# Optimization experiments

Hardware: AMD Instinct MI355X
Metric: run time of the kernel (lower is better)

Reference implementation:

```python
import jax, jax.numpy as jnp
import numpy as np

B, S = 4096, 32
H, NH, HD = 512, 8, 64
NL = 6            # encoder layers
E = 128           # num_experts
CTX = 32          # context_length
LN_EPS = 1e-5


def _ln(x, w, b):
    mu = jnp.mean(x, axis=-1, keepdims=True)
    var = jnp.mean((x - mu) ** 2, axis=-1, keepdims=True)
    return (x - mu) * jax.lax.rsqrt(var + LN_EPS) * w + b


def setup_inputs() -> dict:
    key = jax.random.key(0)
    ks = jax.random.split(key, 20)
    n = lambda k, shape: (jax.random.normal(k, shape, jnp.float32) * 0.02)
    return dict(
        expert_sequence=jax.random.randint(ks[0], (B, S), 0, E),
        layer_id=jax.random.randint(ks[1], (B,), 0, 12),
        expert_table=n(ks[2], (E, H)),
        layer_table=n(ks[3], (12, H)),
        pos_table=n(ks[4], (CTX, H)),
        qkv_w=n(ks[5], (NL, 3 * H, H)), qkv_b=n(ks[6], (NL, 3 * H)),
        out_w=n(ks[7], (NL, H, H)), out_b=n(ks[8], (NL, H)),
        ln1_w=jnp.ones((NL, H)), ln1_b=jnp.zeros((NL, H)),
        ff1_w=n(ks[9], (NL, 2 * H, H)), ff1_b=n(ks[10], (NL, 2 * H)),
        ff2_w=n(ks[11], (NL, H, 2 * H)), ff2_b=n(ks[12], (NL, H)),
        ln2_w=jnp.ones((NL, H)), ln2_b=jnp.zeros((NL, H)),
        head_w=n(ks[13], (NL, E, H)), head_b=n(ks[14], (NL, E)),
        conf_w=n(ks[15], (1, H)), conf_b=jnp.zeros((1,), jnp.float32),
    )


def reference(expert_sequence, layer_id, expert_table, layer_table, pos_table,
              qkv_w, qkv_b, out_w, out_b, ln1_w, ln1_b,
              ff1_w, ff1_b, ff2_w, ff2_b, ln2_w, ln2_b,
              head_w, head_b, conf_w, conf_b):
    Bn, Sn = expert_sequence.shape
    # embedding sum (position defaults to arange % context_length)
    x = (expert_table[expert_sequence]
         + layer_table[layer_id][:, None, :]
         + pos_table[jnp.arange(Sn) % CTX][None, :, :])  # [B,S,H]

    scale = 1.0 / np.float32(np.sqrt(HD))
    for i in range(NL):  # post-norm TransformerEncoderLayer, relu FFN, eval (no dropout)
        qkv = x @ qkv_w[i].T + qkv_b[i]                  # [B,S,3H]
        q, k, v = jnp.split(qkv, 3, axis=-1)
        hview = lambda t: t.reshape(Bn, Sn, NH, HD).transpose(0, 2, 1, 3)
        q, k, v = hview(q), hview(k), hview(v)           # [B,NH,S,HD]
        att = jax.nn.softmax(jnp.einsum('bhqd,bhkd->bhqk', q, k) * scale, axis=-1)
        o = jnp.einsum('bhqk,bhkd->bhqd', att, v).transpose(0, 2, 1, 3).reshape(Bn, Sn, H)
        x = _ln(x + o @ out_w[i].T + out_b[i], ln1_w[i], ln1_b[i])
        ff = jax.nn.relu(x @ ff1_w[i].T + ff1_b[i]) @ ff2_w[i].T + ff2_b[i]
        x = _ln(x + ff, ln2_w[i], ln2_b[i])

    last = x[:, -1, :]                                   # [B,H]
    # head selection: odd layers {1,3,...,11} -> heads 0..5, else fall back to head '1' (idx 0)
    head_idx = jnp.where(layer_id % 2 == 1, (layer_id - 1) // 2, 0)
    prediction = jnp.einsum('bh,beh->be', last, head_w[head_idx]) + head_b[head_idx]
    confidence = jax.nn.sigmoid(last @ conf_w.T + conf_b)  # [B,1]
    return prediction, confidence
```

## Files before the change

### kernel.cpp

```cpp
#include <hip/hip_runtime.h>

typedef __bf16 bf16;
typedef bf16 bf16x8 __attribute__((ext_vector_type(8)));
typedef bf16 bf16x4 __attribute__((ext_vector_type(4)));
typedef float f32x4 __attribute__((ext_vector_type(4)));

#define B_ 4096
#define S_ 32
#define H_ 512
#define NL_ 6
constexpr size_t TOK = (size_t)B_ * S_;

typedef __attribute__((address_space(1))) void* gas_t;
typedef __attribute__((address_space(3))) void* las_t;

__device__ __forceinline__ void async16(bf16* lds, const bf16* g) {
    __builtin_amdgcn_global_load_lds((gas_t)g, (las_t)lds, 16, 0, 0);
}

template<bool RELU>
__global__ __launch_bounds__(256, 2) void gemm_kernel(
    const bf16* __restrict__ A, int lda, const bf16* __restrict__ W,
    const float* __restrict__ bias,
    bf16* C, int N, int K)
{
    __shared__ __align__(16) bf16 As[128 * 64];
    __shared__ __align__(16) bf16 Bs[128 * 64];
    const int tid  = threadIdx.x;
    const int lane = tid & 63, wid = tid >> 6;
    const int m0 = blockIdx.y << 7, n0 = blockIdx.x << 7;
    const int r = lane & 15, quad = lane >> 4;
    const int wm = (wid & 1) << 6, wn = (wid >> 1) << 6;

    f32x4 acc[4][4];
#pragma unroll
    for (int i = 0; i < 4; ++i)
#pragma unroll
        for (int j = 0; j < 4; ++j) acc[i][j] = {0.f, 0.f, 0.f, 0.f};

    const int nkt = K >> 6;
    for (int kt = 0; kt < nkt; ++kt) {
        const int k0 = kt << 6;
#pragma unroll
        for (int p = 0; p < 4; ++p) {
            int q   = p * 256 + tid;
            int row = q >> 3;
            int cs  = q & 7;
            int cg  = cs ^ (row & 7);
            async16(&As[(size_t)(p * 256 + wid * 64) * 8],
                    A + (size_t)(m0 + row) * lda + k0 + cg * 8);
            async16(&Bs[(size_t)(p * 256 + wid * 64) * 8],
                    W + (size_t)(n0 + row) * K + k0 + cg * 8);
        }
        __syncthreads();
#pragma unroll
        for (int ks = 0; ks < 2; ++ks) {
            bf16x8 af[4], bfr[4];
#pragma unroll
            for (int mi = 0; mi < 4; ++mi) {
                int row  = wm + mi * 16 + r;
                int slot = (ks * 4 + quad) ^ (row & 7);
                af[mi] = *(const bf16x8*)&As[row * 64 + slot * 8];
            }
#pragma unroll
            for (int ni = 0; ni < 4; ++ni) {
                int row  = wn + ni * 16 + r;
                int slot = (ks * 4 + quad) ^ (row & 7);
                bfr[ni] = *(const bf16x8*)&Bs[row * 64 + slot * 8];
            }
#pragma unroll
            for (int mi = 0; mi < 4; ++mi)
#pragma unroll
                for (int ni = 0; ni < 4; ++ni)
                    acc[mi][ni] = __builtin_amdgcn_mfma_f32_16x16x32_bf16(
                        af[mi], bfr[ni], acc[mi][ni], 0, 0, 0);
        }
        __syncthreads();
    }
#pragma unroll
    for (int ni = 0; ni < 4; ++ni) {
        int col  = n0 + wn + ni * 16 + r;
        float bv = bias[col];
#pragma unroll
        for (int mi = 0; mi < 4; ++mi) {
            int mrow = m0 + wm + mi * 16 + quad * 4;
#pragma unroll
            for (int rr = 0; rr < 4; ++rr) {
                size_t idx = (size_t)(mrow + rr) * N + col;
                float v = acc[mi][ni][rr] + bv;
                if (RELU) v = fmaxf(v, 0.f);
                C[idx] = (bf16)v;
            }
        }
    }
}

__global__ __launch_bounds__(256, 2) void gemm_ln_kernel(
    const bf16* __restrict__ A, int lda, const bf16* __restrict__ W,
    const float* __restrict__ bias, bf16* x,
    const float* __restrict__ lnw, const float* __restrict__ lnb, int K)
{
    __shared__ __align__(16) bf16 As[64 * 64];
    __shared__ __align__(16) bf16 Ws[512 * 64];
    __shared__ float ps[64][4], ps2[64][4];
    const int tid  = threadIdx.x;
    const int lane = tid & 63, wid = tid >> 6;
    const int m0 = blockIdx.x << 6;
    const int r = lane & 15, quad = lane >> 4;
    const int wn = wid << 7;

    f32x4 acc[4][8];
#pragma unroll
    for (int i = 0; i < 4; ++i)
#pragma unroll
        for (int j = 0; j < 8; ++j) acc[i][j] = {0.f, 0.f, 0.f, 0.f};

    const int nkt = K >> 6;
    for (int kt = 0; kt < nkt; ++kt) {
        const int k0 = kt << 6;
#pragma unroll
        for (int p = 0; p < 2; ++p) {
            int q   = p * 256 + tid;
            int row = q >> 3;
            int cg  = (q & 7) ^ (row & 7);
            async16(&As[(size_t)(p * 256 + wid * 64) * 8],
                    A + (size_t)(m0 + row) * lda + k0 + cg * 8);
        }
#pragma unroll
        for (int p = 0; p < 16; ++p) {
            int q   = p * 256 + tid;
            int row = q >> 3;
            int cg  = (q & 7) ^ (row & 7);
            async16(&Ws[(size_t)(p * 256 + wid * 64) * 8],
                    W + (size_t)row * K + k0 + cg * 8);
        }
        __syncthreads();
#pragma unroll
        for (int ks = 0; ks < 2; ++ks) {
            bf16x8 af[4], wf[8];
#pragma unroll
            for (int mi = 0; mi < 4; ++mi) {
                int row  = mi * 16 + r;
                int slot = (ks * 4 + quad) ^ (row & 7);
                af[mi] = *(const bf16x8*)&As[row * 64 + slot * 8];
            }
#pragma unroll
            for (int ni = 0; ni < 8; ++ni) {
                int row  = wn + ni * 16 + r;
                int slot = (ks * 4 + quad) ^ (row & 7);
                wf[ni] = *(const bf16x8*)&Ws[row * 64 + slot * 8];
            }
#pragma unroll
            for (int mi = 0; mi < 4; ++mi)
#pragma unroll
                for (int ni = 0; ni < 8; ++ni)
                    acc[mi][ni] = __builtin_amdgcn_mfma_f32_16x16x32_bf16(
                        af[mi], wf[ni], acc[mi][ni], 0, 0, 0);
        }
        __syncthreads();
    }

#pragma unroll
    for (int mi = 0; mi < 4; ++mi)
#pragma unroll
        for (int rr = 0; rr < 4; ++rr) {
            int row  = mi * 16 + quad * 4 + rr;
            float s = 0.f, s2 = 0.f;
#pragma unroll
            for (int ni = 0; ni < 8; ++ni) {
                int col = wn + ni * 16 + r;
                float v = acc[mi][ni][rr] + bias[col]
                        + (float)x[(size_t)(m0 + row) * H_ + col];
                acc[mi][ni][rr] = v;
                s += v; s2 += v * v;
            }
#pragma unroll
            for (int off = 8; off >= 1; off >>= 1) {
                s  += __shfl_xor(s,  off, 16);
                s2 += __shfl_xor(s2, off, 16);
            }
            if (r == 0) { ps[row][wid] = s; ps2[row][wid] = s2; }
        }
    __syncthreads();

#pragma unroll
    for (int mi = 0; mi < 4; ++mi)
#pragma unroll
        for (int rr = 0; rr < 4; ++rr) {
            int row = mi * 16 + quad * 4 + rr;
            float s  = ps[row][0] + ps[row][1] + ps[row][2] + ps[row][3];
            float s2 = ps2[row][0] + ps2[row][1] + ps2[row][2] + ps2[row][3];
            float mu  = s * (1.f / 512.f);
            float var = s2 * (1.f / 512.f) - mu * mu;
            float inv = rsqrtf(var + 1e-5f);
#pragma unroll
            for (int ni = 0; ni < 8; ++ni) {
                int col = wn + ni * 16 + r;
                float v = (acc[mi][ni][rr] - mu) * inv * lnw[col] + lnb[col];
                x[(size_t)(m0 + row) * H_ + col] = (bf16)v;
            }
        }
}

__global__ __launch_bounds__(256) void attn_kernel(bf16* qkv)
{
    __shared__ __align__(16) bf16 Pl[4][32][40];
    __shared__ float rs[4][32];
    const int tid = threadIdx.x;
    const int lane = tid & 63, wid = tid >> 6;
    const int pair = blockIdx.x * 4 + wid;
    const int b = pair >> 3, h = pair & 7;
    const int r = lane & 15, quad = lane >> 4;
    bf16* base = qkv + (size_t)b * 32 * 1536 + h * 64;

    bf16x8 aq[2][2], bk[2][2];
#pragma unroll
    for (int t = 0; t < 2; ++t)
#pragma unroll
        for (int ks = 0; ks < 2; ++ks) {
            aq[t][ks] = *(const bf16x8*)(base +       (size_t)(t * 16 + r) * 1536 + ks * 32 + quad * 8);
            bk[t][ks] = *(const bf16x8*)(base + 512 + (size_t)(t * 16 + r) * 1536 + ks * 32 + quad * 8);
        }
    f32x4 sc[2][2];
#pragma unroll
    for (int mt = 0; mt < 2; ++mt)
#pragma unroll
        for (int nt = 0; nt < 2; ++nt) sc[mt][nt] = {0.f, 0.f, 0.f, 0.f};
#pragma unroll
    for (int mt = 0; mt < 2; ++mt)
#pragma unroll
        for (int nt = 0; nt < 2; ++nt)
#pragma unroll
            for (int ks = 0; ks < 2; ++ks)
                sc[mt][nt] = __builtin_amdgcn_mfma_f32_16x16x32_bf16(
                    aq[mt][ks], bk[nt][ks], sc[mt][nt], 0, 0, 0);

#pragma unroll
    for (int mt = 0; mt < 2; ++mt)
#pragma unroll
        for (int rr = 0; rr < 4; ++rr) {
            int i = mt * 16 + quad * 4 + rr;
            float v0 = sc[mt][0][rr] * 0.125f;
            float v1 = sc[mt][1][rr] * 0.125f;
            float mx = fmaxf(v0, v1);
#pragma unroll
            for (int off = 8; off >= 1; off >>= 1) mx = fmaxf(mx, __shfl_xor(mx, off, 16));
            float e0 = __expf(v0 - mx), e1 = __expf(v1 - mx);
            float s = e0 + e1;
#pragma unroll
            for (int off = 8; off >= 1; off >>= 1) s += __shfl_xor(s, off, 16);
            Pl[wid][i][r]      = (bf16)e0;
            Pl[wid][i][r + 16] = (bf16)e1;
            if (r == 0) rs[wid][i] = s;
        }
    __syncthreads();

    const bf16* vb = base + 1024;
    bf16x8 av[4];
#pragma unroll
    for (int mt = 0; mt < 4; ++mt)
#pragma unroll
        for (int jj = 0; jj < 8; ++jj)
            av[mt][jj] = vb[(size_t)(quad * 8 + jj) * 1536 + mt * 16 + r];
    bf16x8 bp[2];
#pragma unroll
    for (int nt = 0; nt < 2; ++nt)
        bp[nt] = *(const bf16x8*)&Pl[wid][nt * 16 + r][quad * 8];
    f32x4 oc[4][2];
#pragma unroll
    for (int mt = 0; mt < 4; ++mt)
#pragma unroll
        for (int nt = 0; nt < 2; ++nt) oc[mt][nt] = {0.f, 0.f, 0.f, 0.f};
#pragma unroll
    for (int mt = 0; mt < 4; ++mt)
#pragma unroll
        for (int nt = 0; nt < 2; ++nt)
            oc[mt][nt] = __builtin_amdgcn_mfma_f32_16x16x32_bf16(av[mt], bp[nt], oc[mt][nt], 0, 0, 0);

    float inv0 = 1.f / rs[wid][r];
    float inv1 = 1.f / rs[wid][r + 16];
    bf16* ob = base;
#pragma unroll
    for (int mt = 0; mt < 4; ++mt)
#pragma unroll
        for (int nt = 0; nt < 2; ++nt) {
            int i = nt * 16 + r;
            float invv = nt ? inv1 : inv0;
            bf16x4 pk;
#pragma unroll
            for (int rr = 0; rr < 4; ++rr) pk[rr] = (bf16)(oc[mt][nt][rr] * invv);
            *(bf16x4*)(ob + (size_t)i * 1536 + mt * 16 + quad * 4) = pk;
        }
}

__global__ __launch_bounds__(256) void embed_kernel(
    const int* __restrict__ seq, const int* __restrict__ lid,
    const float* __restrict__ et, const float* __restrict__ lt, const float* __restrict__ pt,
    bf16* __restrict__ x, int t0)
{
    const int rowg = t0 + blockIdx.x;
    const int b = rowg >> 5, s = rowg & 31;
    const int e = seq[rowg];
    const int l = lid[b];
    const float* pe = et + (size_t)e * H_;
    const float* pl = lt + (size_t)l * H_;
    const float* pp = pt + (size_t)s * H_;
    for (int c = threadIdx.x; c < H_; c += 256)
        x[(size_t)blockIdx.x * H_ + c] = (bf16)(pe[c] + pl[c] + pp[c]);
}

__global__ __launch_bounds__(256) void cvt_kernel(const float* __restrict__ in, bf16* __restrict__ out, int n)
{
    int i = blockIdx.x * 256 + threadIdx.x;
    if (i < n) out[i] = (bf16)in[i];
}

__global__ __launch_bounds__(256) void head_kernel(
    const bf16* __restrict__ x, const int* __restrict__ lid,
    const float* __restrict__ hw, const float* __restrict__ hb,
    const float* __restrict__ cw, const float* __restrict__ cb, float* __restrict__ out, int b0)
{
    __shared__ float last[512];
    __shared__ float part[256];
    const int bl = blockIdx.x, tid = threadIdx.x;
    const int b = b0 + bl;
    const size_t row = (size_t)bl * 32 + 31;
    for (int c = tid; c < 512; c += 256) last[c] = (float)x[row * 512 + c];
    __syncthreads();
    int l = lid[b];
    int hidx = (l & 1) ? ((l - 1) >> 1) : 0;
    int e = tid & 127, half = tid >> 7;
    const float* wr = hw + ((size_t)hidx * 128 + e) * 512 + half * 256;
    float s = 0.f;
    for (int k = 0; k < 256; ++k) s += last[half * 256 + k] * wr[k];
    part[tid] = s;
    __syncthreads();
    if (tid < 128) out[(size_t)b * 128 + tid] = part[tid] + part[tid + 128] + hb[hidx * 128 + tid];
    if (tid >= 128 && tid < 192) {
        int ln = tid - 128;
        float cs = 0.f;
#pragma unroll
        for (int k = 0; k < 8; ++k) cs += last[ln * 8 + k] * cw[ln * 8 + k];
#pragma unroll
        for (int off = 32; off >= 1; off >>= 1) cs += __shfl_xor(cs, off, 64);
        if (ln == 0) out[(size_t)B_ * 128 + b] = 1.f / (1.f + __expf(-(cs + cb[0])));
    }
}

extern "C" void kernel_launch(void* const* d_in, const int* in_sizes, int n_in,
                              void* d_out, int out_size, void* d_ws, size_t ws_size,
                              hipStream_t stream)
{
    const int*   seq          = (const int*)d_in[0];
    const int*   lid          = (const int*)d_in[1];
    const float* expert_table = (const float*)d_in[2];
    const float* layer_table  = (const float*)d_in[3];
    const float* pos_table    = (const float*)d_in[4];
    const float* qkv_w        = (const float*)d_in[5];
    const float* qkv_b        = (const float*)d_in[6];
    const float* out_w        = (const float*)d_in[7];
    const float* out_b        = (const float*)d_in[8];
    const float* ln1_w        = (const float*)d_in[9];
    const float* ln1_b        = (const float*)d_in[10];
    const float* ff1_w        = (const float*)d_in[11];
    const float* ff1_b        = (const float*)d_in[12];
    const float* ff2_w        = (const float*)d_in[13];
    const float* ff2_b        = (const float*)d_in[14];
    const float* ln2_w        = (const float*)d_in[15];
    const float* ln2_b        = (const float*)d_in[16];
    const float* head_w       = (const float*)d_in[17];
    const float* head_b       = (const float*)d_in[18];
    const float* conf_w       = (const float*)d_in[19];
    const float* conf_b       = (const float*)d_in[20];
    float* out = (float*)d_out;

    constexpr size_t NWQ = (size_t)NL_ * 1536 * 512;
    constexpr size_t NWO = (size_t)NL_ * 512 * 512;
    constexpr size_t NW1 = (size_t)NL_ * 1024 * 512;
    constexpr size_t NW2 = (size_t)NL_ * 512 * 1024;
    constexpr size_t WELEM = NWQ + NWO + NW1 + NW2;
    int nchunk = 1;
    while (nchunk < 1024) {
        size_t ct = TOK / (size_t)nchunk;
        size_t need = WELEM * 2 + ct * 2048 * 2;
        if (need <= ws_size) break;
        nchunk <<= 1;
    }
    const size_t chunkTok = TOK / (size_t)nchunk;

    bf16* wq = (bf16*)d_ws;
    bf16* wo = wq + NWQ;
    bf16* w1 = wo + NWO;
    bf16* w2 = w1 + NW1;
    bf16* xb = w2 + NW2;
    bf16* qb = xb + chunkTok * 512;

    cvt_kernel<<<(int)((NWQ + 255) / 256), 256, 0, stream>>>(qkv_w, wq, (int)NWQ);
    cvt_kernel<<<(int)((NWO + 255) / 256), 256, 0, stream>>>(out_w, wo, (int)NWO);
    cvt_kernel<<<(int)((NW1 + 255) / 256), 256, 0, stream>>>(ff1_w, w1, (int)NW1);
    cvt_kernel<<<(int)((NW2 + 255) / 256), 256, 0, stream>>>(ff2_w, w2, (int)NW2);

    const int mg = (int)(chunkTok / 128);
    const int lg = (int)(chunkTok / 64);
    for (int c = 0; c < nchunk; ++c) {
        const int t0 = (int)(c * chunkTok);
        embed_kernel<<<(int)chunkTok, 256, 0, stream>>>(seq, lid, expert_table, layer_table,
                                                        pos_table, xb, t0);
        for (int i = 0; i < NL_; ++i) {
            gemm_kernel<false><<<dim3(12, mg), 256, 0, stream>>>(
                xb, 512, wq + (size_t)i * 1536 * 512, qkv_b + i * 1536, qb, 1536, 512);
            attn_kernel<<<(int)(chunkTok / 16), 256, 0, stream>>>(qb);
            gemm_ln_kernel<<<lg, 256, 0, stream>>>(
                qb, 1536, wo + (size_t)i * 512 * 512, out_b + i * 512, xb,
                ln1_w + i * 512, ln1_b + i * 512, 512);
            gemm_kernel<true><<<dim3(8, mg), 256, 0, stream>>>(
                xb, 512, w1 + (size_t)i * 1024 * 512, ff1_b + i * 1024, qb, 1024, 512);
            gemm_ln_kernel<<<lg, 256, 0, stream>>>(
                qb, 1024, w2 + (size_t)i * 512 * 1024, ff2_b + i * 512, xb,
                ln2_w + i * 512, ln2_b + i * 512, 1024);
        }
        head_kernel<<<(int)(chunkTok / 32), 256, 0, stream>>>(xb, lid, head_w, head_b,
                                                              conf_w, conf_b, out, t0 / 32);
    }
}
```

Measured before the change: 5.605 ms.

## Fuse attention with output projection and LayerNorm; add XCD-aware GEMM block swizzle

Attention, the output projection GEMM and the first residual+LayerNorm now run in one kernel. Each 512-thread block handles one sequence, with one wave per head. The attention output stays in swizzled LDS instead of being written to and re-read from global memory, and one kernel launch per layer is removed. The projection weights are read straight from global memory per block with no LDS tiling, so Wo traffic rises, and the per-block LDS use and thread count change occupancy. Separately, the GEMM remaps block indices so that consecutive M tiles land on different XCDs, aiming for better L2 reuse of the weights.

Result: slower. 5.955 ms (+6.2%).

```diff
diff --git a/kernel.cpp b/kernel.cpp
--- a/kernel.cpp
+++ b/kernel.cpp
@@ -28,7 +28,17 @@
     __shared__ __align__(16) bf16 Bs[128 * 64];
     const int tid  = threadIdx.x;
     const int lane = tid & 63, wid = tid >> 6;
-    const int m0 = blockIdx.y << 7, n0 = blockIdx.x << 7;
+    int m_idx, n_idx;
+    {
+        const int nb = gridDim.x, mgd = gridDim.y;
+        if ((mgd & 7) == 0) {
+            int id  = blockIdx.y * nb + blockIdx.x;
+            int xcd = id & 7, j = id >> 3;
+            n_idx = j % nb;
+            m_idx = (j / nb) * 8 + xcd;
+        } else { m_idx = blockIdx.y; n_idx = blockIdx.x; }
+    }
+    const int m0 = m_idx << 7, n0 = n_idx << 7;
     const int r = lane & 15, quad = lane >> 4;
     const int wm = (wid & 1) << 6, wn = (wid >> 1) << 6;
 
@@ -45,8 +55,7 @@
         for (int p = 0; p < 4; ++p) {
             int q   = p * 256 + tid;
             int row = q >> 3;
-            int cs  = q & 7;
-            int cg  = cs ^ (row & 7);
+            int cg  = (q & 7) ^ (row & 7);
             async16(&As[(size_t)(p * 256 + wid * 64) * 8],
                     A + (size_t)(m0 + row) * lda + k0 + cg * 8);
             async16(&Bs[(size_t)(p * 256 + wid * 64) * 8],
@@ -202,16 +211,20 @@
         }
 }
 
-__global__ __launch_bounds__(256) void attn_kernel(bf16* qkv)
-{
-    __shared__ __align__(16) bf16 Pl[4][32][40];
-    __shared__ float rs[4][32];
+__global__ __launch_bounds__(512, 4) void attn_proj_ln_kernel(
+    const bf16* __restrict__ qkv, const bf16* __restrict__ Wo,
+    const float* __restrict__ bias, bf16* x,
+    const float* __restrict__ lnw, const float* __restrict__ lnb)
+{
+    __shared__ __align__(16) bf16 Ol[32 * 512];
+    __shared__ __align__(16) bf16 Pl[8][32][40];
+    __shared__ float rs[8][32];
+    __shared__ float ps[32][8], ps2[32][8];
     const int tid = threadIdx.x;
-    const int lane = tid & 63, wid = tid >> 6;
-    const int pair = blockIdx.x * 4 + wid;
-    const int b = pair >> 3, h = pair & 7;
+    const int lane = tid & 63, h = tid >> 6;
+    const int b = blockIdx.x;
     const int r = lane & 15, quad = lane >> 4;
-    bf16* base = qkv + (size_t)b * 32 * 1536 + h * 64;
+    const bf16* base = qkv + (size_t)b * 32 * 1536 + h * 64;
 
     bf16x8 aq[2][2], bk[2][2];
 #pragma unroll
@@ -249,11 +262,10 @@
             float s = e0 + e1;
 #pragma unroll
             for (int off = 8; off >= 1; off >>= 1) s += __shfl_xor(s, off, 16);
-            Pl[wid][i][r]      = (bf16)e0;
-            Pl[wid][i][r + 16] = (bf16)e1;
-            if (r == 0) rs[wid][i] = s;
-        }
-    __syncthreads();
+            Pl[h][i][r]      = (bf16)e0;
+            Pl[h][i][r + 16] = (bf16)e1;
+            if (r == 0) rs[h][i] = s;
+        }
 
     const bf16* vb = base + 1024;
     bf16x8 av[4];
@@ -265,7 +277,7 @@
     bf16x8 bp[2];
 #pragma unroll
     for (int nt = 0; nt < 2; ++nt)
-        bp[nt] = *(const bf16x8*)&Pl[wid][nt * 16 + r][quad * 8];
+        bp[nt] = *(const bf16x8*)&Pl[h][nt * 16 + r][quad * 8];
     f32x4 oc[4][2];
 #pragma unroll
     for (int mt = 0; mt < 4; ++mt)
@@ -277,19 +289,90 @@
         for (int nt = 0; nt < 2; ++nt)
             oc[mt][nt] = __builtin_amdgcn_mfma_f32_16x16x32_bf16(av[mt], bp[nt], oc[mt][nt], 0, 0, 0);
 
-    float inv0 = 1.f / rs[wid][r];
-    float inv1 = 1.f / rs[wid][r + 16];
-    bf16* ob = base;
+    float inv0 = 1.f / rs[h][r];
+    float inv1 = 1.f / rs[h][r + 16];
 #pragma unroll
     for (int mt = 0; mt < 4; ++mt)
 #pragma unroll
         for (int nt = 0; nt < 2; ++nt) {
-            int i = nt * 16 + r;
+            int iq = nt * 16 + r;
             float invv = nt ? inv1 : inv0;
             bf16x4 pk;
 #pragma unroll
             for (int rr = 0; rr < 4; ++rr) pk[rr] = (bf16)(oc[mt][nt][rr] * invv);
-            *(bf16x4*)(ob + (size_t)i * 1536 + mt * 16 + quad * 4) = pk;
+            int colbase = h * 64 + mt * 16 + quad * 4;
+            int chunk = colbase >> 3, inner = colbase & 7;
+            *(bf16x4*)&Ol[iq * 512 + ((chunk ^ (iq & 7)) << 3) + inner] = pk;
+        }
+    __syncthreads();
+
+    f32x4 acc[2][4];
+#pragma unroll
+    for (int i = 0; i < 2; ++i)
+#pragma unroll
+        for (int j = 0; j < 4; ++j) acc[i][j] = {0.f, 0.f, 0.f, 0.f};
+#pragma unroll
+    for (int ks = 0; ks < 16; ++ks) {
+        bf16x8 af[2], wf[4];
+#pragma unroll
+        for (int mi = 0; mi < 2; ++mi) {
+            int row = mi * 16 + r;
+            int chunk = ks * 4 + quad;
+            af[mi] = *(const bf16x8*)&Ol[row * 512 + ((chunk ^ (row & 7)) << 3)];
+        }
+#pragma unroll
+        for (int ni = 0; ni < 4; ++ni) {
+            int wrow = h * 64 + ni * 16 + r;
+            wf[ni] = *(const bf16x8*)&Wo[(size_t)wrow * 512 + ks * 32 + quad * 8];
+        }
+#pragma unroll
+        for (int mi = 0; mi < 2; ++mi)
+#pragma unroll
+            for (int ni = 0; ni < 4; ++ni)
+                acc[mi][ni] = __builtin_amdgcn_mfma_f32_16x16x32_bf16(
+                    af[mi], wf[ni], acc[mi][ni], 0, 0, 0);
+    }
+
+    const size_t xrow0 = (size_t)b * 32;
+#pragma unroll
+    for (int mi = 0; mi < 2; ++mi)
+#pragma unroll
+        for (int rr = 0; rr < 4; ++rr) {
+            int row = mi * 16 + quad * 4 + rr;
+            float s = 0.f, s2 = 0.f;
+#pragma unroll
+            for (int ni = 0; ni < 4; ++ni) {
+                int col = h * 64 + ni * 16 + r;
+                float v = acc[mi][ni][rr] + bias[col]
+                        + (float)x[(xrow0 + row) * H_ + col];
+                acc[mi][ni][rr] = v;
+                s += v; s2 += v * v;
+            }
+#pragma unroll
+            for (int off = 8; off >= 1; off >>= 1) {
+                s  += __shfl_xor(s,  off, 16);
+                s2 += __shfl_xor(s2, off, 16);
+            }
+            if (r == 0) { ps[row][h] = s; ps2[row][h] = s2; }
+        }
+    __syncthreads();
+#pragma unroll
+    for (int mi = 0; mi < 2; ++mi)
+#pragma unroll
+        for (int rr = 0; rr < 4; ++rr) {
+            int row = mi * 16 + quad * 4 + rr;
+            float s = 0.f, s2 = 0.f;
+#pragma unroll
+            for (int w = 0; w < 8; ++w) { s += ps[row][w]; s2 += ps2[row][w]; }
+            float mu  = s * (1.f / 512.f);
+            float var = s2 * (1.f / 512.f) - mu * mu;
+            float inv = rsqrtf(var + 1e-5f);
+#pragma unroll
+            for (int ni = 0; ni < 4; ++ni) {
+                int col = h * 64 + ni * 16 + r;
+                float v = (acc[mi][ni][rr] - mu) * inv * lnw[col] + lnb[col];
+                x[(xrow0 + row) * H_ + col] = (bf16)v;
+            }
         }
 }
 
@@ -402,6 +485,7 @@
 
     const int mg = (int)(chunkTok / 128);
     const int lg = (int)(chunkTok / 64);
+    const int ag = (int)(chunkTok / 32);
     for (int c = 0; c < nchunk; ++c) {
         const int t0 = (int)(c * chunkTok);
         embed_kernel<<<(int)chunkTok, 256, 0, stream>>>(seq, lid, expert_table, layer_table,
@@ -409,10 +493,9 @@
         for (int i = 0; i < NL_; ++i) {
             gemm_kernel<false><<<dim3(12, mg), 256, 0, stream>>>(
                 xb, 512, wq + (size_t)i * 1536 * 512, qkv_b + i * 1536, qb, 1536, 512);
-            attn_kernel<<<(int)(chunkTok / 16), 256, 0, stream>>>(qb);
-            gemm_ln_kernel<<<lg, 256, 0, stream>>>(
-                qb, 1536, wo + (size_t)i * 512 * 512, out_b + i * 512, xb,
-                ln1_w + i * 512, ln1_b + i * 512, 512);
+            attn_proj_ln_kernel<<<ag, 512, 0, stream>>>(
+                qb, wo + (size_t)i * 512 * 512, out_b + i * 512, xb,
+                ln1_w + i * 512, ln1_b + i * 512);
             gemm_kernel<true><<<dim3(8, mg), 256, 0, stream>>>(
                 xb, 512, w1 + (size_t)i * 1024 * 512, ff1_b + i * 1024, qb, 1024, 512);
             gemm_ln_kernel<<<lg, 256, 0, stream>>>(
```
